# Kernel tuning notes

Measured on AMD Instinct MI355X. Metric: run time of the kernel, lower is better.

## Reference

```python
import jax, jax.numpy as jnp
import numpy as np

N = 100000   # nodes
E = 1600000  # edges (avg degree 16)
G = 128      # graphs in batch
D_IN, D_HID, D_OUT = 128, 256, 128


def setup_inputs() -> dict:
    key = jax.random.key(0)
    ks = jax.random.split(key, 12)
    x = jax.random.normal(ks[0], (N, D_IN), jnp.float32)
    edge_index = jax.random.randint(ks[1], (2, E), 0, N, dtype=jnp.int64)
    batch = jnp.sort(jax.random.randint(ks[2], (N,), 0, G, dtype=jnp.int64))

    def lin(k, i, o):
        return jax.random.normal(k, (i, o), jnp.float32) / np.float32(np.sqrt(i))

    return {
        "x": x, "edge_index": edge_index, "batch": batch,
        "W0": lin(ks[3], D_IN, D_HID),  "b0": jnp.zeros((D_HID,), jnp.float32),
        "W1": lin(ks[4], D_HID, D_HID), "b1": jnp.zeros((D_HID,), jnp.float32),
        "W2": lin(ks[5], D_HID, D_OUT), "b2": jnp.zeros((D_OUT,), jnp.float32),
        "Wf1": lin(ks[6], D_OUT, D_HID), "bf1": jnp.zeros((D_HID,), jnp.float32),
        "Wf2": lin(ks[7], D_HID, 1),     "bf2": jnp.zeros((1,), jnp.float32),
    }


def reference(x, edge_index, batch, W0, b0, W1, b1, W2, b2, Wf1, bf1, Wf2, bf2):
    n = x.shape[0]
    # GCNConv: add self-loops, symmetric deg^{-1/2} normalization,
    # linear transform, scatter-add aggregation, bias added after aggregation
    # (matches PyG GCNConv defaults; dropout is identity in eval mode).
    loop = jnp.arange(n, dtype=edge_index.dtype)
    src = jnp.concatenate([edge_index[0], loop])
    dst = jnp.concatenate([edge_index[1], loop])
    deg = jax.ops.segment_sum(jnp.ones_like(dst, x.dtype), dst, num_segments=n)
    dinv = jax.lax.rsqrt(jnp.maximum(deg, 1.0))  # deg >= 1 after self-loops
    norm = dinv[src] * dinv[dst]                 # [E+N]

    def conv(h, W, b):
        h = h @ W                                # [N, out]
        msg = h[src] * norm[:, None]             # gather + normalize
        return jax.ops.segment_sum(msg, dst, num_segments=n) + b

    h = jax.nn.relu(conv(x, W0, b0))
    h = jax.nn.relu(conv(h, W1, b1))
    h = conv(h, W2, b2)                          # last conv, no relu

    # global mean pool over graphs
    s = jax.ops.segment_sum(h, batch, num_segments=G)
    cnt = jax.ops.segment_sum(jnp.ones((n,), h.dtype), batch, num_segments=G)
    g = s / jnp.maximum(cnt, 1.0)[:, None]       # [G, D_OUT]

    out = jax.nn.relu(g @ Wf1 + bf1)
    return jax.nn.sigmoid(out @ Wf2 + bf2)       # [G, 1]
```

## Files before the change

### kernel.cpp

```cpp
#include <hip/hip_runtime.h>
#include <hip/hip_bf16.h>

typedef __hip_bfloat16 hbf16;
typedef __attribute__((ext_vector_type(8))) short short8;
typedef __attribute__((ext_vector_type(4))) float f32x4;
typedef __attribute__((ext_vector_type(2))) float f32x2;
typedef __attribute__((ext_vector_type(2))) unsigned uint2v;
typedef __attribute__((ext_vector_type(4))) float f32x4v;

static __device__ __forceinline__ float bits2f(unsigned short u) {
  return __uint_as_float(((unsigned)u) << 16);
}
static __device__ __forceinline__ unsigned short f2bits(float f) {
  hbf16 h = __float2bfloat16(f);
  return *reinterpret_cast<unsigned short*>(&h);
}


#define BSH2 9
#define CHUNK 8192

__global__ __launch_bounds__(256) void k_bcnt(
    const int* __restrict__ dst, int e, int nbuk,
    int* __restrict__ bcnt, int* __restrict__ blockOff) {
  __shared__ int hist[1024];
  int t = threadIdx.x;
  int e0 = blockIdx.x * CHUNK;
  int e1 = min(e, e0 + CHUNK);
  for (int b = t; b < nbuk; b += 256) hist[b] = 0;
  __syncthreads();
  for (int i = e0 + t; i < e1; i += 256)
    atomicAdd(&hist[__builtin_nontemporal_load(&dst[i]) >> BSH2], 1);
  __syncthreads();
  for (int b = t; b < nbuk; b += 256) {
    int h = hist[b];
    blockOff[(size_t)blockIdx.x * nbuk + b] = h ? atomicAdd(&bcnt[b], h) : 0;
  }
}

__global__ __launch_bounds__(1024) void k_scanB(
    const int* __restrict__ bcnt, int nbuk, int e,
    int* __restrict__ bstart, int* __restrict__ rowStart, int n) {
  __shared__ int s[1024];
  int t = threadIdx.x;
  int v = (t < nbuk) ? bcnt[t] : 0;
  s[t] = v;
  __syncthreads();
  for (int off = 1; off < 1024; off <<= 1) {
    int x = (t >= off) ? s[t - off] : 0;
    __syncthreads();
    s[t] += x;
    __syncthreads();
  }
  if (t < nbuk) bstart[t] = s[t] - v;
  if (t == 0) { bstart[nbuk] = e; rowStart[n] = e; }
}

__global__ __launch_bounds__(256) void k_partA(
    const int* __restrict__ src, const int* __restrict__ dst, int e, int nbuk,
    const int* __restrict__ bstart, const int* __restrict__ blockOff,
    unsigned* __restrict__ staging) {
  __shared__ int pos[1024];
  int t = threadIdx.x;
  int e0 = blockIdx.x * CHUNK;
  int e1 = min(e, e0 + CHUNK);
  for (int b = t; b < nbuk; b += 256)
    pos[b] = bstart[b] + blockOff[(size_t)blockIdx.x * nbuk + b];
  __syncthreads();
  for (int i = e0 + t; i < e1; i += 256) {
    int d = __builtin_nontemporal_load(&dst[i]);
    int sv = __builtin_nontemporal_load(&src[i]);
    int b = d >> BSH2;
    int r = atomicAdd(&pos[b], 1);
    staging[r] = (unsigned)sv | ((unsigned)(d & 511) << 23);
  }
}

__global__ __launch_bounds__(512) void k_bucket_csr(
    const unsigned* __restrict__ staging, const int* __restrict__ bstart,
    int* __restrict__ rowStart, float* __restrict__ dinv, int* __restrict__ csr, int N) {
  __shared__ int hist[512];
  __shared__ int s[512];
  __shared__ int cnt[512];
  int b = blockIdx.x, t = threadIdx.x;
  int es = bstart[b], ee = bstart[b + 1];
  hist[t] = 0;
  __syncthreads();
  for (int i = es + t; i < ee; i += 512)
    atomicAdd(&hist[staging[i] >> 23], 1);
  __syncthreads();
  s[t] = hist[t];
  __syncthreads();
  for (int off = 1; off < 512; off <<= 1) {
    int x = (t >= off) ? s[t - off] : 0;
    __syncthreads();
    s[t] += x;
    __syncthreads();
  }
  int gpos = es + s[t] - hist[t];
  cnt[t] = gpos;
  int d = (b << BSH2) + t;
  if (d < N) {
    rowStart[d] = gpos;
    dinv[d] = rsqrtf((float)(hist[t] + 1));
  }
  __syncthreads();
  for (int i = es + t; i < ee; i += 512) {
    unsigned w = staging[i];
    int pos = atomicAdd(&cnt[w >> 23], 1);
    csr[pos] = (int)(w & 0x7fffffu);
  }
}

__global__ void k_wt_all(const float* __restrict__ W0, const float* __restrict__ W1,
                         const float* __restrict__ W2, unsigned short* __restrict__ W0t,
                         unsigned short* __restrict__ W1t, unsigned short* __restrict__ W2t) {
  int i = blockIdx.x * blockDim.x + threadIdx.x;
  const float* W; unsigned short* Wt; int K, M, idx;
  if (i < 32768)       { W = W0; Wt = W0t; K = 128; M = 256; idx = i; }
  else if (i < 98304)  { W = W1; Wt = W1t; K = 256; M = 256; idx = i - 32768; }
  else if (i < 131072) { W = W2; Wt = W2t; K = 256; M = 128; idx = i - 98304; }
  else return;
  int m = idx / K, k = idx - m * K;
  Wt[idx] = f2bits(W[k * M + m]);
}

__global__ void k_cast_fp8(const float* __restrict__ x, const float* __restrict__ dinv,
                           unsigned* __restrict__ y, int n4) {
  int i = blockIdx.x * blockDim.x + threadIdx.x;
  if (i < n4) {
    float s = 16.f * dinv[i >> 5];
    f32x4v v = __builtin_nontemporal_load(reinterpret_cast<const f32x4v*>(x) + i);
    unsigned q = 0;
    q = __builtin_amdgcn_cvt_pk_fp8_f32(v[0] * s, v[1] * s, q, false);
    q = __builtin_amdgcn_cvt_pk_fp8_f32(v[2] * s, v[3] * s, q, true);
    y[i] = q;
  }
}


template<int VPL>
static __device__ __forceinline__ unsigned agg8_load(
    const void* __restrict__ h8, int idx, int lane) {
  if constexpr (VPL == 4)
    return reinterpret_cast<const unsigned*>(h8)[(size_t)idx * 64 + lane];
  else
    return (unsigned)reinterpret_cast<const unsigned short*>(h8)[(size_t)idx * 64 + lane];
}

template<int VPL>
static __device__ __forceinline__ void agg8_add(unsigned v, float* acc) {
  f32x2 lo = __builtin_amdgcn_cvt_pk_f32_fp8(v, false);
  acc[0] += lo[0]; acc[1] += lo[1];
  if constexpr (VPL == 4) {
    f32x2 hi = __builtin_amdgcn_cvt_pk_f32_fp8(v, true);
    acc[2] += hi[0]; acc[3] += hi[1];
  }
}

template<int VPL, int U>
static __device__ __forceinline__ void agg8_chunk(
    const void* __restrict__ h8, const int* __restrict__ csr,
    int k, int lane, float* acc) {
  unsigned v[U];
#pragma unroll
  for (int u = 0; u < U; ++u) {
    int idx = __builtin_nontemporal_load(&csr[k + u]);
    v[u] = agg8_load<VPL>(h8, idx, lane);
  }
#pragma unroll
  for (int u = 0; u < U; ++u) agg8_add<VPL>(v[u], acc);
}

template<int D, int BIAS>
__global__ __launch_bounds__(256) void aggregate_f8(
    const void* __restrict__ h8, const int* __restrict__ csr,
    const int* __restrict__ rowStart, const float* __restrict__ dinv,
    const float* __restrict__ bias, unsigned short* __restrict__ out, int N) {
  constexpr int VPL = D / 64;
  int lane = threadIdx.x & 63;
  int d = (blockIdx.x * 256 + threadIdx.x) >> 6;
  if (d >= N) return;
  int rs = __builtin_amdgcn_readfirstlane(rowStart[d]);
  int re = __builtin_amdgcn_readfirstlane(rowStart[d + 1]);

  float acc[VPL] = {};
  agg8_add<VPL>(agg8_load<VPL>(h8, d, lane), acc);

  int k = rs;
  for (; k + 16 <= re; k += 16) agg8_chunk<VPL, 16>(h8, csr, k, lane, acc);
  if (k + 8 <= re) { agg8_chunk<VPL, 8>(h8, csr, k, lane, acc); k += 8; }
  if (k + 4 <= re) { agg8_chunk<VPL, 4>(h8, csr, k, lane, acc); k += 4; }
  for (; k < re; ++k) {
    int idx = __builtin_nontemporal_load(&csr[k]);
    agg8_add<VPL>(agg8_load<VPL>(h8, idx, lane), acc);
  }

  float dv = dinv[d] * 0.0625f;
  unsigned o[VPL / 2];
#pragma unroll
  for (int j = 0; j < VPL / 2; ++j) {
    float v0 = acc[2 * j] * dv, v1 = acc[2 * j + 1] * dv;
    if (BIAS) {
      f32x2 bv = *reinterpret_cast<const f32x2*>(bias + lane * VPL + 2 * j);
      v0 += bv[0]; v1 += bv[1];
    }
    o[j] = (unsigned)f2bits(v0) | ((unsigned)f2bits(v1) << 16);
  }
  unsigned* ob = reinterpret_cast<unsigned*>(out) + (size_t)d * (D / 2) + lane * (VPL / 2);
  if constexpr (VPL == 4) {
    *reinterpret_cast<uint2*>(ob) = make_uint2(o[0], o[1]);
  } else {
    *ob = o[0];
  }
}


#define GLD16(g, l) __builtin_amdgcn_global_load_lds(                         \
    (const __attribute__((address_space(1))) void*)(g),                       \
    (__attribute__((address_space(3))) void*)(l), 16, 0, 0)

template<int K, int EPI>
__global__ __launch_bounds__(256) void gemm_mfma(
    const unsigned short* __restrict__ A, const unsigned short* __restrict__ Bt,
    const float* __restrict__ bias, const float* __restrict__ dinv,
    void* __restrict__ Cv, int N, int M) {
  __shared__ __align__(16) char smem[32768];
  char* lA = smem;
  char* lB = smem + 16384;
  int tid = threadIdx.x, lane = tid & 63, wid = tid >> 6;
  int rowBase = blockIdx.x * 128, colBase = blockIdx.y * 128;
  int wr = (wid >> 1) * 64, wc = (wid & 1) * 64;

  f32x4 zero = {0.f, 0.f, 0.f, 0.f};
  f32x4 acc[4][4];
#pragma unroll
  for (int m = 0; m < 4; ++m)
#pragma unroll
    for (int n = 0; n < 4; ++n) acc[m][n] = zero;

  const char* Ab = (const char*)A;
  const char* Bb = (const char*)Bt;

  for (int k0 = 0; k0 < K; k0 += 64) {
#pragma unroll
    for (int r = 0; r < 4; ++r) {
      int pbase = r * 256 + wid * 64;
      int p = pbase + lane;
      int row = p >> 3;
      int offg = ((p & 7) * 16) ^ ((row & 7) << 4);
      int ga = min(rowBase + row, N - 1);
      GLD16(Ab + (size_t)ga * (K * 2) + k0 * 2 + offg, lA + pbase * 16);
      int gb = colBase + row;
      GLD16(Bb + (size_t)gb * (K * 2) + k0 * 2 + offg, lB + pbase * 16);
    }
    __syncthreads();
    int l15 = lane & 15, lhi = lane >> 4;
#pragma unroll
    for (int kk = 0; kk < 2; ++kk) {
      short8 af[4], bfr[4];
      int koff = kk * 64 + lhi * 16;
#pragma unroll
      for (int m = 0; m < 4; ++m) {
        int row = wr + m * 16 + l15;
        af[m] = *reinterpret_cast<const short8*>(lA + row * 128 + (koff ^ ((row & 7) << 4)));
      }
#pragma unroll
      for (int n = 0; n < 4; ++n) {
        int col = wc + n * 16 + l15;
        bfr[n] = *reinterpret_cast<const short8*>(lB + col * 128 + (koff ^ ((col & 7) << 4)));
      }
#pragma unroll
      for (int m = 0; m < 4; ++m)
#pragma unroll
        for (int n = 0; n < 4; ++n)
          acc[m][n] = __builtin_amdgcn_mfma_f32_16x16x32_bf16(af[m], bfr[n], acc[m][n], 0, 0, 0);
    }
    __syncthreads();
  }

  int l15 = lane & 15, lhi = lane >> 4;
  float dvv[4][4];
  if (EPI == 2 || EPI == 3) {
#pragma unroll
    for (int m = 0; m < 4; ++m)
#pragma unroll
      for (int r = 0; r < 4; ++r) {
        int row = rowBase + wr + m * 16 + lhi * 4 + r;
        dvv[m][r] = (row < N) ? 16.f * dinv[row] : 1.f;
      }
  }
#pragma unroll
  for (int n = 0; n < 4; ++n) {
    int col = colBase + wc + n * 16 + l15;
    float bv = (EPI == 1 || EPI == 2) ? bias[col] : 0.f;
#pragma unroll
    for (int m = 0; m < 4; ++m) {
#pragma unroll
      for (int r = 0; r < 4; ++r) {
        int row = rowBase + wr + m * 16 + lhi * 4 + r;
        if (row < N) {
          float v = acc[m][n][r] + bv;
          if (EPI == 1 || EPI == 2) v = fmaxf(v, 0.f);
          if (EPI == 1) {
            ((unsigned short*)Cv)[(size_t)row * M + col] = f2bits(v);
          } else {
            v *= dvv[m][r];
            unsigned pk = __builtin_amdgcn_cvt_pk_fp8_f32(v, v, 0, false);
            ((unsigned char*)Cv)[(size_t)row * M + col] = (unsigned char)pk;
          }
        }
      }
    }
  }
}


__global__ void graph_bounds(const int* batch, int n, int g_cnt, int* gstart) {
  int g = blockIdx.x * blockDim.x + threadIdx.x;
  if (g > g_cnt) return;
  int lo = 0, hi = n;
  while (lo < hi) {
    int mid = (lo + hi) >> 1;
    if (batch[mid] < g) lo = mid + 1; else hi = mid;
  }
  gstart[g] = lo;
}

__global__ void pool_partial(const unsigned short* __restrict__ h,
                             const int* __restrict__ batch, int N, float* gbuf) {
  int per = (N + gridDim.x - 1) / gridDim.x;
  int lo = blockIdx.x * per;
  int hi = min(N, lo + per);
  if (lo >= hi) return;
  int t = threadIdx.x;
  int cur = batch[lo];
  float acc = 0.f;
  for (int i = lo; i < hi; ++i) {
    int g = batch[i];
    if (g != cur) {
      atomicAdd(&gbuf[cur * 128 + t], acc);
      acc = 0.f;
      cur = g;
    }
    acc += bits2f(__builtin_nontemporal_load(&h[(size_t)i * 128 + t]));
  }
  atomicAdd(&gbuf[cur * 128 + t], acc);
}


__global__ __launch_bounds__(256) void mlp(const float* __restrict__ gbuf,
                                           const int* __restrict__ gstart,
                                           const float* __restrict__ Wf1,
                                           const float* __restrict__ bf1,
                                           const float* __restrict__ Wf2,
                                           const float* __restrict__ bf2,
                                           float* __restrict__ out) {
  __shared__ float gs[128];
  __shared__ float hid[256];
  int b = blockIdx.x, t = threadIdx.x;
  float inv = 1.f / (float)max(gstart[b + 1] - gstart[b], 1);
  if (t < 128) gs[t] = gbuf[b * 128 + t] * inv;
  __syncthreads();
  float acc = bf1[t];
  for (int k = 0; k < 128; ++k) acc += gs[k] * Wf1[k * 256 + t];
  acc = fmaxf(acc, 0.f);
  hid[t] = acc * Wf2[t];
  __syncthreads();
  for (int s2 = 128; s2 > 0; s2 >>= 1) {
    if (t < s2) hid[t] += hid[t + s2];
    __syncthreads();
  }
  if (t == 0) out[b] = 1.f / (1.f + expf(-(hid[0] + bf2[0])));
}


extern "C" void kernel_launch(void* const* d_in, const int* in_sizes, int n_in,
                              void* d_out, int out_size, void* d_ws, size_t ws_size,
                              hipStream_t stream) {
  const float* x   = (const float*)d_in[0];
  const int* ei    = (const int*)d_in[1];
  const int* batch = (const int*)d_in[2];
  const float* W0  = (const float*)d_in[3];
  const float* b0  = (const float*)d_in[4];
  const float* W1  = (const float*)d_in[5];
  const float* b1  = (const float*)d_in[6];
  const float* W2  = (const float*)d_in[7];
  const float* b2  = (const float*)d_in[8];
  const float* Wf1 = (const float*)d_in[9];
  const float* bf1 = (const float*)d_in[10];
  const float* Wf2 = (const float*)d_in[11];
  const float* bf2 = (const float*)d_in[12];
  float* out = (float*)d_out;

  const int DIN = 128, DH = 256, DOUT = 128, G = 128;
  const int N = in_sizes[0] / DIN;
  const int E = in_sizes[1] / 2;
  const int* src = ei;
  const int* dst = ei + E;
  const int NBUK = (N + 511) >> BSH2;
  const int NCHUNK = (E + CHUNK - 1) / CHUNK;

  char* p = (char*)d_ws;
  auto alloc = [&](size_t bytes) {
    char* r = p;
    p += (bytes + 255) & ~(size_t)255;
    return r;
  };
  int* bcnt     = (int*)alloc((size_t)NBUK * 4);
  int* blockOff = (int*)alloc((size_t)NCHUNK * NBUK * 4);
  int* bstart   = (int*)alloc((size_t)(NBUK + 1) * 4);
  int* rowStart = (int*)alloc((size_t)(N + 1) * 4);
  float* dinv   = (float*)alloc((size_t)N * 4);
  int* csr      = (int*)alloc((size_t)E * 4);
  int* gstart   = (int*)alloc((size_t)(G + 1) * 4);
  float* gbuf   = (float*)alloc((size_t)G * DOUT * 4);
  unsigned short* W0t = (unsigned short*)alloc((size_t)DIN * DH * 2);
  unsigned short* W1t = (unsigned short*)alloc((size_t)DH * DH * 2);
  unsigned short* W2t = (unsigned short*)alloc((size_t)DH * DOUT * 2);
  char* S1 = (char*)alloc((size_t)N * DH * 2);
  char* S2 = (char*)alloc((size_t)N * DH * 2);

  unsigned* staging = (unsigned*)S2;

  unsigned*       xb8    = (unsigned*)S1;
  unsigned short* agg0   = (unsigned short*)S2;
  unsigned char*  h1s8   = (unsigned char*)S1;
  unsigned short* agg1   = (unsigned short*)S2;
  unsigned short* h2     = (unsigned short*)S1;
  unsigned char*  t2s8   = (unsigned char*)S2;
  unsigned short* aggout = (unsigned short*)S1;

  const int tb = 256;
  hipMemsetAsync(bcnt, 0, (size_t)NBUK * 4, stream);
  hipMemsetAsync(gbuf, 0, (size_t)G * DOUT * 4, stream);

  k_bcnt<<<NCHUNK, 256, 0, stream>>>(dst, E, NBUK, bcnt, blockOff);
  k_scanB<<<1, 1024, 0, stream>>>(bcnt, NBUK, E, bstart, rowStart, N);
  k_partA<<<NCHUNK, 256, 0, stream>>>(src, dst, E, NBUK, bstart, blockOff, staging);
  k_bucket_csr<<<NBUK, 512, 0, stream>>>(staging, bstart, rowStart, dinv, csr, N);

  k_wt_all<<<(131072 + tb - 1) / tb, tb, 0, stream>>>(W0, W1, W2, W0t, W1t, W2t);

  int n4 = N * DIN / 4;
  k_cast_fp8<<<(n4 + tb - 1) / tb, tb, 0, stream>>>(x, dinv, xb8, n4);

  int gx = (N + 127) / 128;
  int ga = (N + 3) / 4;

  aggregate_f8<128, 0><<<ga, 256, 0, stream>>>(xb8, csr, rowStart, dinv, nullptr, agg0, N);
  gemm_mfma<128, 2><<<dim3(gx, 2), 256, 0, stream>>>(agg0, W0t, b0, dinv, h1s8, N, DH);

  aggregate_f8<256, 0><<<ga, 256, 0, stream>>>(h1s8, csr, rowStart, dinv, nullptr, agg1, N);
  gemm_mfma<256, 1><<<dim3(gx, 2), 256, 0, stream>>>(agg1, W1t, b1, nullptr, h2, N, DH);

  gemm_mfma<256, 3><<<dim3(gx, 1), 256, 0, stream>>>(h2, W2t, nullptr, dinv, t2s8, N, DOUT);
  aggregate_f8<128, 1><<<ga, 256, 0, stream>>>(t2s8, csr, rowStart, dinv, b2, aggout, N);

  graph_bounds<<<1, 256, 0, stream>>>(batch, N, G, gstart);
  pool_partial<<<1000, 128, 0, stream>>>(aggout, batch, N, gbuf);
  mlp<<<G, 256, 0, stream>>>(gbuf, gstart, Wf1, bf1, Wf2, bf2, out);
}
```

Baseline: 385.4 us.

## Store all intermediate activations as fp8 and dequantize A tiles in GEMM

Every intermediate buffer (aggregation outputs, h2, final aggregation) now holds fp8 with a 16x scale folded in, where before several were bf16. The GEMM A-operand is loaded as fp8 through ordinary global loads and dequantized to bf16 into swizzled LDS, replacing the direct global-to-LDS copies. The aim is to halve the memory traffic of the aggregation writes, the GEMM reads and the pooling reads. The cost is extra conversion ALU work in the GEMM load path and lower numeric precision across more stages.

```diff
diff --git a/kernel.cpp b/kernel.cpp
--- a/kernel.cpp
+++ b/kernel.cpp
@@ -5,7 +5,6 @@
 typedef __attribute__((ext_vector_type(8))) short short8;
 typedef __attribute__((ext_vector_type(4))) float f32x4;
 typedef __attribute__((ext_vector_type(2))) float f32x2;
-typedef __attribute__((ext_vector_type(2))) unsigned uint2v;
 typedef __attribute__((ext_vector_type(4))) float f32x4v;
 
 static __device__ __forceinline__ float bits2f(unsigned short u) {
@@ -176,7 +175,7 @@
 __global__ __launch_bounds__(256) void aggregate_f8(
     const void* __restrict__ h8, const int* __restrict__ csr,
     const int* __restrict__ rowStart, const float* __restrict__ dinv,
-    const float* __restrict__ bias, unsigned short* __restrict__ out, int N) {
+    const float* __restrict__ bias, void* __restrict__ outv, int N) {
   constexpr int VPL = D / 64;
   int lane = threadIdx.x & 63;
   int d = (blockIdx.x * 256 + threadIdx.x) >> 6;
@@ -196,22 +195,21 @@
     agg8_add<VPL>(agg8_load<VPL>(h8, idx, lane), acc);
   }
 
-  float dv = dinv[d] * 0.0625f;
-  unsigned o[VPL / 2];
-#pragma unroll
-  for (int j = 0; j < VPL / 2; ++j) {
-    float v0 = acc[2 * j] * dv, v1 = acc[2 * j + 1] * dv;
-    if (BIAS) {
-      f32x2 bv = *reinterpret_cast<const f32x2*>(bias + lane * VPL + 2 * j);
-      v0 += bv[0]; v1 += bv[1];
-    }
-    o[j] = (unsigned)f2bits(v0) | ((unsigned)f2bits(v1) << 16);
-  }
-  unsigned* ob = reinterpret_cast<unsigned*>(out) + (size_t)d * (D / 2) + lane * (VPL / 2);
+  float dv = dinv[d];
+  float v[VPL];
+#pragma unroll
+  for (int j = 0; j < VPL; ++j) {
+    v[j] = acc[j] * dv;
+    if (BIAS) v[j] += 16.f * bias[lane * VPL + j];
+  }
   if constexpr (VPL == 4) {
-    *reinterpret_cast<uint2*>(ob) = make_uint2(o[0], o[1]);
+    unsigned q = 0;
+    q = __builtin_amdgcn_cvt_pk_fp8_f32(v[0], v[1], q, false);
+    q = __builtin_amdgcn_cvt_pk_fp8_f32(v[2], v[3], q, true);
+    reinterpret_cast<unsigned*>(outv)[(size_t)d * 64 + lane] = q;
   } else {
-    *ob = o[0];
+    unsigned q = __builtin_amdgcn_cvt_pk_fp8_f32(v[0], v[1], 0, false);
+    reinterpret_cast<unsigned short*>(outv)[(size_t)d * 64 + lane] = (unsigned short)q;
   }
 }
 
@@ -220,11 +218,27 @@
     (const __attribute__((address_space(1))) void*)(g),                       \
     (__attribute__((address_space(3))) void*)(l), 16, 0, 0)
 
+static __device__ __forceinline__ void dq_store(uint4 v, char* lA, int r, int c8) {
+  unsigned ow[8];
+#pragma unroll
+  for (int j = 0; j < 4; ++j) {
+    unsigned w = (&v.x)[j];
+    f32x2 lo = __builtin_amdgcn_cvt_pk_f32_fp8(w, false);
+    f32x2 hi = __builtin_amdgcn_cvt_pk_f32_fp8(w, true);
+    ow[2 * j]     = (unsigned)f2bits(lo[0]) | ((unsigned)f2bits(lo[1]) << 16);
+    ow[2 * j + 1] = (unsigned)f2bits(hi[0]) | ((unsigned)f2bits(hi[1]) << 16);
+  }
+  int s0 = (c8 * 2) ^ (r & 7);
+  int s1 = (c8 * 2 + 1) ^ (r & 7);
+  *reinterpret_cast<uint4*>(lA + r * 128 + s0 * 16) = make_uint4(ow[0], ow[1], ow[2], ow[3]);
+  *reinterpret_cast<uint4*>(lA + r * 128 + s1 * 16) = make_uint4(ow[4], ow[5], ow[6], ow[7]);
+}
+
 template<int K, int EPI>
 __global__ __launch_bounds__(256) void gemm_mfma(
-    const unsigned short* __restrict__ A, const unsigned short* __restrict__ Bt,
+    const unsigned char* __restrict__ A8, const unsigned short* __restrict__ Bt,
     const float* __restrict__ bias, const float* __restrict__ dinv,
-    void* __restrict__ Cv, int N, int M) {
+    unsigned char* __restrict__ C8, int N, int M) {
   __shared__ __align__(16) char smem[32768];
   char* lA = smem;
   char* lB = smem + 16384;
@@ -239,8 +253,9 @@
 #pragma unroll
     for (int n = 0; n < 4; ++n) acc[m][n] = zero;
 
-  const char* Ab = (const char*)A;
   const char* Bb = (const char*)Bt;
+  int ar = tid >> 1, ah = tid & 1;
+  int ga = min(rowBase + ar, N - 1);
 
   for (int k0 = 0; k0 < K; k0 += 64) {
 #pragma unroll
@@ -249,10 +264,15 @@
       int p = pbase + lane;
       int row = p >> 3;
       int offg = ((p & 7) * 16) ^ ((row & 7) << 4);
-      int ga = min(rowBase + row, N - 1);
-      GLD16(Ab + (size_t)ga * (K * 2) + k0 * 2 + offg, lA + pbase * 16);
       int gb = colBase + row;
       GLD16(Bb + (size_t)gb * (K * 2) + k0 * 2 + offg, lB + pbase * 16);
+    }
+    {
+      const unsigned char* Ap = A8 + (size_t)ga * K + k0 + ah * 32;
+      uint4 va = *reinterpret_cast<const uint4*>(Ap);
+      uint4 vb = *reinterpret_cast<const uint4*>(Ap + 16);
+      dq_store(va, lA, ar, ah * 2);
+      dq_store(vb, lA, ar, ah * 2 + 1);
     }
     __syncthreads();
     int l15 = lane & 15, lhi = lane >> 4;
@@ -287,28 +307,31 @@
 #pragma unroll
       for (int r = 0; r < 4; ++r) {
         int row = rowBase + wr + m * 16 + lhi * 4 + r;
-        dvv[m][r] = (row < N) ? 16.f * dinv[row] : 1.f;
+        float dq = (row < N) ? dinv[row] : 1.f;
+        dvv[m][r] = (EPI == 2) ? 16.f * dq : dq;
       }
   }
 #pragma unroll
   for (int n = 0; n < 4; ++n) {
     int col = colBase + wc + n * 16 + l15;
-    float bv = (EPI == 1 || EPI == 2) ? bias[col] : 0.f;
+    float bv = (EPI == 2 || EPI == 4) ? bias[col] : 0.f;
 #pragma unroll
     for (int m = 0; m < 4; ++m) {
 #pragma unroll
       for (int r = 0; r < 4; ++r) {
         int row = rowBase + wr + m * 16 + lhi * 4 + r;
         if (row < N) {
-          float v = acc[m][n][r] + bv;
-          if (EPI == 1 || EPI == 2) v = fmaxf(v, 0.f);
-          if (EPI == 1) {
-            ((unsigned short*)Cv)[(size_t)row * M + col] = f2bits(v);
+          float a16 = acc[m][n][r];
+          float v;
+          if (EPI == 2) {
+            v = fmaxf(fmaf(a16, 0.0625f, bv), 0.f) * dvv[m][r];
+          } else if (EPI == 3) {
+            v = a16 * dvv[m][r];
           } else {
-            v *= dvv[m][r];
-            unsigned pk = __builtin_amdgcn_cvt_pk_fp8_f32(v, v, 0, false);
-            ((unsigned char*)Cv)[(size_t)row * M + col] = (unsigned char)pk;
+            v = fmaxf(a16 + 16.f * bv, 0.f);
           }
+          unsigned pk = __builtin_amdgcn_cvt_pk_fp8_f32(v, v, 0, false);
+          C8[(size_t)row * M + col] = (unsigned char)pk;
         }
       }
     }
@@ -327,7 +350,7 @@
   gstart[g] = lo;
 }
 
-__global__ void pool_partial(const unsigned short* __restrict__ h,
+__global__ void pool_partial(const unsigned char* __restrict__ h8,
                              const int* __restrict__ batch, int N, float* gbuf) {
   int per = (N + gridDim.x - 1) / gridDim.x;
   int lo = blockIdx.x * per;
@@ -343,7 +366,9 @@
       acc = 0.f;
       cur = g;
     }
-    acc += bits2f(__builtin_nontemporal_load(&h[(size_t)i * 128 + t]));
+    unsigned b = (unsigned)__builtin_nontemporal_load(&h8[(size_t)i * 128 + t]);
+    f32x2 lo2 = __builtin_amdgcn_cvt_pk_f32_fp8(b, false);
+    acc += lo2[0];
   }
   atomicAdd(&gbuf[cur * 128 + t], acc);
 }
@@ -359,7 +384,7 @@
   __shared__ float gs[128];
   __shared__ float hid[256];
   int b = blockIdx.x, t = threadIdx.x;
-  float inv = 1.f / (float)max(gstart[b + 1] - gstart[b], 1);
+  float inv = 0.0625f / (float)max(gstart[b + 1] - gstart[b], 1);
   if (t < 128) gs[t] = gbuf[b * 128 + t] * inv;
   __syncthreads();
   float acc = bf1[t];
@@ -423,13 +448,13 @@
 
   unsigned* staging = (unsigned*)S2;
 
-  unsigned*       xb8    = (unsigned*)S1;
-  unsigned short* agg0   = (unsigned short*)S2;
-  unsigned char*  h1s8   = (unsigned char*)S1;
-  unsigned short* agg1   = (unsigned short*)S2;
-  unsigned short* h2     = (unsigned short*)S1;
-  unsigned char*  t2s8   = (unsigned char*)S2;
-  unsigned short* aggout = (unsigned short*)S1;
+  unsigned*      xb8     = (unsigned*)S1;
+  unsigned char* agg0_8  = (unsigned char*)S2;
+  unsigned char* h1s8    = (unsigned char*)S1;
+  unsigned char* agg1_8  = (unsigned char*)S2;
+  unsigned char* h2_8    = (unsigned char*)S1;
+  unsigned char* t2s8    = (unsigned char*)S2;
+  unsigned char* aggout8 = (unsigned char*)S1;
 
   const int tb = 256;
   hipMemsetAsync(bcnt, 0, (size_t)NBUK * 4, stream);
@@ -448,16 +473,16 @@
   int gx = (N + 127) / 128;
   int ga = (N + 3) / 4;
 
-  aggregate_f8<128, 0><<<ga, 256, 0, stream>>>(xb8, csr, rowStart, dinv, nullptr, agg0, N);
-  gemm_mfma<128, 2><<<dim3(gx, 2), 256, 0, stream>>>(agg0, W0t, b0, dinv, h1s8, N, DH);
-
-  aggregate_f8<256, 0><<<ga, 256, 0, stream>>>(h1s8, csr, rowStart, dinv, nullptr, agg1, N);
-  gemm_mfma<256, 1><<<dim3(gx, 2), 256, 0, stream>>>(agg1, W1t, b1, nullptr, h2, N, DH);
-
-  gemm_mfma<256, 3><<<dim3(gx, 1), 256, 0, stream>>>(h2, W2t, nullptr, dinv, t2s8, N, DOUT);
-  aggregate_f8<128, 1><<<ga, 256, 0, stream>>>(t2s8, csr, rowStart, dinv, b2, aggout, N);
+  aggregate_f8<128, 0><<<ga, 256, 0, stream>>>(xb8, csr, rowStart, dinv, nullptr, agg0_8, N);
+  gemm_mfma<128, 2><<<dim3(gx, 2), 256, 0, stream>>>(agg0_8, W0t, b0, dinv, h1s8, N, DH);
+
+  aggregate_f8<256, 0><<<ga, 256, 0, stream>>>(h1s8, csr, rowStart, dinv, nullptr, agg1_8, N);
+  gemm_mfma<256, 4><<<dim3(gx, 2), 256, 0, stream>>>(agg1_8, W1t, b1, nullptr, h2_8, N, DH);
+
+  gemm_mfma<256, 3><<<dim3(gx, 1), 256, 0, stream>>>(h2_8, W2t, nullptr, dinv, t2s8, N, DOUT);
+  aggregate_f8<128, 1><<<ga, 256, 0, stream>>>(t2s8, csr, rowStart, dinv, b2, aggout8, N);
 
   graph_bounds<<<1, 256, 0, stream>>>(batch, N, G, gstart);
-  pool_partial<<<1000, 128, 0, stream>>>(aggout, batch, N, gbuf);
+  pool_partial<<<1000, 128, 0, stream>>>(aggout8, batch, N, gbuf);
   mlp<<<G, 256, 0, stream>>>(gbuf, gstart, Wf1, bf1, Wf2, bf2, out);
 }
```

Measured after the change: 373.6 us. -3.1%, faster.
